# Optimization experiments

Hardware: AMD Instinct MI355X
Metric: run time of the kernel (lower is better)

The kernel has to match this reference:

```python
import jax, jax.numpy as jnp
import numpy as np

N_NODES = 100000
N_EDGES = 250000
D_NODE = 128
D_EDGE = 128
D_HID = 512
LN_EPS = 1e-5


def setup_inputs() -> dict:
    key = jax.random.key(0)
    ks = jax.random.split(key, 8)
    src_node_features = jax.random.normal(ks[0], (N_NODES, D_NODE), dtype=jnp.float32)
    dst_node_features = jax.random.normal(ks[1], (N_NODES, D_NODE), dtype=jnp.float32)
    edge_features = jax.random.normal(ks[2], (N_EDGES, D_EDGE), dtype=jnp.float32)
    src_indices = jax.random.randint(ks[3], (N_EDGES,), 0, N_NODES, dtype=jnp.int64 if jax.config.jax_enable_x64 else jnp.int32)
    dst_indices = jax.random.randint(ks[4], (N_EDGES,), 0, N_NODES, dtype=jnp.int64 if jax.config.jax_enable_x64 else jnp.int32)
    d_in = 2 * D_NODE + D_EDGE
    W1 = jax.random.normal(ks[5], (d_in, D_HID), dtype=jnp.float32) * (1.0 / np.sqrt(d_in))
    b1 = jnp.zeros((D_HID,), dtype=jnp.float32)
    W2 = jax.random.normal(ks[6], (D_HID, D_EDGE), dtype=jnp.float32) * (1.0 / np.sqrt(D_HID))
    b2 = jnp.zeros((D_EDGE,), dtype=jnp.float32)
    ln_gamma = jnp.ones((D_EDGE,), dtype=jnp.float32)
    ln_beta = jnp.zeros((D_EDGE,), dtype=jnp.float32)
    return {
        "src_node_features": src_node_features,
        "dst_node_features": dst_node_features,
        "edge_features": edge_features,
        "src_indices": src_indices,
        "dst_indices": dst_indices,
        "W1": W1, "b1": b1, "W2": W2, "b2": b2,
        "ln_gamma": ln_gamma, "ln_beta": ln_beta,
    }


def reference(src_node_features, dst_node_features, edge_features,
              src_indices, dst_indices, W1, b1, W2, b2, ln_gamma, ln_beta):
    # Gather node features per-edge (irregular access)
    s = src_node_features[src_indices]          # [E, D_NODE]
    d = dst_node_features[dst_indices]          # [E, D_NODE]
    x = jnp.concatenate([s, d, edge_features], axis=-1)  # [E, 2*D_NODE + D_EDGE]
    # MeshGraphMLP: Linear -> SiLU -> Linear -> LayerNorm
    h = jax.nn.silu(x @ W1 + b1)                # [E, D_HID]
    y = h @ W2 + b2                             # [E, D_EDGE]
    mu = jnp.mean(y, axis=-1, keepdims=True)
    var = jnp.var(y, axis=-1, keepdims=True)
    y = (y - mu) * jax.lax.rsqrt(var + LN_EPS) * ln_gamma + ln_beta
    # Residual add
    return y + edge_features
```

## Files before the change

kernel.cpp:

```cpp
#include <hip/hip_runtime.h>
#include <hip/hip_bf16.h>


typedef __bf16 bf16;
typedef __bf16 bf16x8 __attribute__((ext_vector_type(8)));
typedef float f32x4 __attribute__((ext_vector_type(4)));

#define E_TOT 250000
#define N_NODES 100000
#define ET 64
#define NBLK ((E_TOT + ET - 1) / ET)

__global__ __launch_bounds__(256) void pack_weights(const float* __restrict__ W1,
                                                    const float* __restrict__ W2,
                                                    bf16* __restrict__ W1p,
                                                    bf16* __restrict__ W2p) {
  int tid = blockIdx.x * blockDim.x + threadIdx.x;
  if (tid < 384 * 512) {
    int k = tid >> 9;
    int n = tid & 511;
    int kb = k >> 5, quad = (k >> 3) & 3, j = k & 7;
    W1p[(((kb * 4 + quad) * 512) + n) * 8 + j] = (bf16)W1[tid];
  }
  if (tid < 512 * 128) {
    int k = tid >> 7;
    int n = tid & 127;
    int kc = k >> 5, quad = (k >> 3) & 3, j = k & 7;
    W2p[(((kc * 4 + quad) * 128) + n) * 8 + j] = (bf16)W2[tid];
  }
}

__global__ __launch_bounds__(512, 4)
void edge_mlp_kernel(const float* __restrict__ srcf,
                     const float* __restrict__ dstf,
                     const float* __restrict__ edgef,
                     const int* __restrict__ sidx,
                     const int* __restrict__ didx,
                     const bf16* __restrict__ W1p,
                     const bf16* __restrict__ W2p,
                     const float* __restrict__ b1p,
                     const float* __restrict__ b2p,
                     const float* __restrict__ gp,
                     const float* __restrict__ bp,
                     float* __restrict__ out) {
  __shared__ __align__(16) bf16 Xs[48 * 512];
  __shared__ __align__(16) bf16 Hs[16 * 512];

  const int tid = threadIdx.x;
  const int w = tid >> 6;
  const int lane = tid & 63;
  const int l15 = lane & 15;
  const int quad = lane >> 4;
  const int h = w >> 2;
  const int q = w & 3;
  const long base = (long)blockIdx.x * ET;

  {
    const int mt = w & 3;
    const int half = w >> 2;
    int e = (int)base + mt * 16 + l15;
    int ec = e < E_TOT ? e : (E_TOT - 1);
    int si = sidx[ec];
    int di = didx[ec];
    si = si < 0 ? 0 : (si >= N_NODES ? N_NODES - 1 : si);
    di = di < 0 ? 0 : (di >= N_NODES ? N_NODES - 1 : di);
    const float* rs = srcf + (long)si * 128;
    const float* rd = dstf + (long)di * 128;
    const float* re = edgef + (long)ec * 128;
#pragma unroll
    for (int kk = 0; kk < 6; ++kk) {
      int kb = half * 6 + kk;
      const float* rowp = (kb < 4) ? rs : ((kb < 8) ? rd : re);
      int off = ((kb & 3) << 5) + (quad << 3);
      float4 v0 = *(const float4*)(rowp + off);
      float4 v1 = *(const float4*)(rowp + off + 4);
      bf16x8 vb;
      vb[0] = (bf16)v0.x; vb[1] = (bf16)v0.y; vb[2] = (bf16)v0.z; vb[3] = (bf16)v0.w;
      vb[4] = (bf16)v1.x; vb[5] = (bf16)v1.y; vb[6] = (bf16)v1.z; vb[7] = (bf16)v1.w;
      *(bf16x8*)(&Xs[(mt * 12 + kb) * 512 + lane * 8]) = vb;
    }
  }

  float b2v[2], gv[2], bv[2];
#pragma unroll
  for (int t = 0; t < 2; ++t) {
    int n2 = q * 32 + t * 16 + l15;
    b2v[t] = b2p[n2];
    gv[t] = gp[n2];
    bv[t] = bp[n2];
  }

  f32x4 acc2[2][2];
#pragma unroll
  for (int i = 0; i < 2; ++i)
#pragma unroll
    for (int t = 0; t < 2; ++t)
      acc2[i][t] = (f32x4){0.f, 0.f, 0.f, 0.f};

  __syncthreads();

  for (int nc = 0; nc < 4; ++nc) {
    f32x4 acc1[2][2];
#pragma unroll
    for (int i = 0; i < 2; ++i)
#pragma unroll
      for (int t = 0; t < 2; ++t)
        acc1[i][t] = (f32x4){0.f, 0.f, 0.f, 0.f};

    float b1v[2];
#pragma unroll
    for (int t = 0; t < 2; ++t)
      b1v[t] = b1p[nc * 128 + q * 32 + t * 16 + l15];

#pragma unroll
    for (int kb = 0; kb < 12; ++kb) {
      const bf16* wp = W1p + (((long)(kb * 4 + quad) * 512) + nc * 128 + q * 32) * 8;
      bf16x8 b[2];
      b[0] = *(const bf16x8*)(wp + l15 * 8);
      b[1] = *(const bf16x8*)(wp + (16 + l15) * 8);
      bf16x8 a[2];
#pragma unroll
      for (int i = 0; i < 2; ++i)
        a[i] = *(const bf16x8*)(&Xs[((h * 2 + i) * 12 + kb) * 512 + lane * 8]);
#pragma unroll
      for (int i = 0; i < 2; ++i)
#pragma unroll
        for (int t = 0; t < 2; ++t)
          acc1[i][t] =
              __builtin_amdgcn_mfma_f32_16x16x32_bf16(a[i], b[t], acc1[i][t], 0, 0, 0);
    }

    __syncthreads();

#pragma unroll
    for (int i = 0; i < 2; ++i)
#pragma unroll
      for (int t = 0; t < 2; ++t) {
        int pos0 = ((t * 2 + (l15 >> 3)) * 128) + (quad * 4) * 8 + (l15 & 7);
        bf16* hp = &Hs[((h * 2 + i) * 4 + q) * 512 + pos0];
#pragma unroll
        for (int r = 0; r < 4; ++r) {
          float vv = acc1[i][t][r] + b1v[t];
          float s = vv / (1.0f + __expf(-vv));
          hp[r * 8] = (bf16)s;
        }
      }
    __syncthreads();

#pragma unroll
    for (int kb2 = 0; kb2 < 4; ++kb2) {
      const bf16* wp =
          W2p + (((long)((nc * 4 + kb2) * 4 + quad) * 128) + q * 32) * 8;
      bf16x8 b[2];
      b[0] = *(const bf16x8*)(wp + l15 * 8);
      b[1] = *(const bf16x8*)(wp + (16 + l15) * 8);
      bf16x8 a[2];
#pragma unroll
      for (int i = 0; i < 2; ++i)
        a[i] = *(const bf16x8*)(&Hs[((h * 2 + i) * 4 + kb2) * 512 + lane * 8]);
#pragma unroll
      for (int i = 0; i < 2; ++i)
#pragma unroll
        for (int t = 0; t < 2; ++t)
          acc2[i][t] =
              __builtin_amdgcn_mfma_f32_16x16x32_bf16(a[i], b[t], acc2[i][t], 0, 0, 0);
    }
  }

  __syncthreads();

  float* psum = (float*)Hs;
  float* psq = psum + 256;
  float* pmu = psq + 256;
  float* prs = pmu + 64;

#pragma unroll
  for (int i = 0; i < 2; ++i) {
#pragma unroll
    for (int r = 0; r < 4; ++r) {
      float v0 = acc2[i][0][r] + b2v[0];
      float v1 = acc2[i][1][r] + b2v[1];
      float s = v0 + v1;
      float ss = v0 * v0 + v1 * v1;
#pragma unroll
      for (int mk = 8; mk >= 1; mk >>= 1) {
        s += __shfl_xor(s, mk, 64);
        ss += __shfl_xor(ss, mk, 64);
      }
      if (l15 == 0) {
        int row = (h * 2 + i) * 16 + quad * 4 + r;
        psum[row * 4 + q] = s;
        psq[row * 4 + q] = ss;
      }
    }
  }
  __syncthreads();
  if (tid < 64) {
    float s = psum[tid * 4] + psum[tid * 4 + 1] + psum[tid * 4 + 2] + psum[tid * 4 + 3];
    float ss = psq[tid * 4] + psq[tid * 4 + 1] + psq[tid * 4 + 2] + psq[tid * 4 + 3];
    float mu = s * (1.0f / 128.0f);
    float var = fmaxf(ss * (1.0f / 128.0f) - mu * mu, 0.0f);
    pmu[tid] = mu;
    prs[tid] = rsqrtf(var + 1e-5f);
  }
  __syncthreads();

#pragma unroll
  for (int i = 0; i < 2; ++i) {
#pragma unroll
    for (int r = 0; r < 4; ++r) {
      int m = (h * 2 + i) * 16 + quad * 4 + r;
      long e = base + m;
      if (e >= E_TOT) continue;
      float mu = pmu[m];
      float rsg = prs[m];
#pragma unroll
      for (int t = 0; t < 2; ++t) {
        int n2 = q * 32 + t * 16 + l15;
        float v = acc2[i][t][r] + b2v[t];
        int posE = ((t * 2 + (l15 >> 3)) * 128) + (quad * 4 + r) * 8 + (l15 & 7);
        float ev = (float)Xs[((h * 2 + i) * 12 + 8 + q) * 512 + posE];
        float y = (v - mu) * rsg * gv[t] + bv[t] + ev;
        out[e * 128 + n2] = y;
      }
    }
  }
}

extern "C" void kernel_launch(void* const* d_in, const int* in_sizes, int n_in,
                              void* d_out, int out_size, void* d_ws, size_t ws_size,
                              hipStream_t stream) {
  const float* srcf = (const float*)d_in[0];
  const float* dstf = (const float*)d_in[1];
  const float* edgef = (const float*)d_in[2];
  const int* sidx = (const int*)d_in[3];
  const int* didx = (const int*)d_in[4];
  const float* W1 = (const float*)d_in[5];
  const float* b1 = (const float*)d_in[6];
  const float* W2 = (const float*)d_in[7];
  const float* b2 = (const float*)d_in[8];
  const float* g = (const float*)d_in[9];
  const float* be = (const float*)d_in[10];
  float* out = (float*)d_out;

  bf16* W1p = (bf16*)d_ws;
  bf16* W2p = W1p + 384 * 512;

  pack_weights<<<(384 * 512 + 255) / 256, 256, 0, stream>>>(W1, W2, W1p, W2p);

  edge_mlp_kernel<<<NBLK, 512, 0, stream>>>(srcf, dstf, edgef, sidx, didx,
                                            W1p, W2p, b1, b2, g, be, out);
}
```

Measured before the change: 527.7 us.

## Double-buffer hidden tile in LDS and prefetch weight fragments ahead of MFMA

The hidden-activation LDS buffer is doubled so consecutive chunks alternate buffers, which lets one of the two barriers per chunk be removed. Weight fragments for both GEMMs are now loaded two k-steps ahead in a register ping-pong, so global load latency can overlap the MFMA work. This costs extra LDS, which may reduce occupancy, and extra registers for the prefetched fragments.

```diff
diff --git a/kernel.cpp b/kernel.cpp
--- a/kernel.cpp
+++ b/kernel.cpp
@@ -44,7 +44,7 @@
                      const float* __restrict__ bp,
                      float* __restrict__ out) {
   __shared__ __align__(16) bf16 Xs[48 * 512];
-  __shared__ __align__(16) bf16 Hs[16 * 512];
+  __shared__ __align__(16) bf16 Hs[2 * 16 * 512];
 
   const int tid = threadIdx.x;
   const int w = tid >> 6;
@@ -100,6 +100,8 @@
   __syncthreads();
 
   for (int nc = 0; nc < 4; ++nc) {
+    bf16* hbuf = &Hs[(nc & 1) * 16 * 512];
+
     f32x4 acc1[2][2];
 #pragma unroll
     for (int i = 0; i < 2; ++i)
@@ -112,12 +114,16 @@
     for (int t = 0; t < 2; ++t)
       b1v[t] = b1p[nc * 128 + q * 32 + t * 16 + l15];
 
+    bf16x8 bB[2][2];
+#pragma unroll
+    for (int p = 0; p < 2; ++p) {
+      const bf16* wp = W1p + (((long)(p * 4 + quad) * 512) + nc * 128 + q * 32) * 8;
+      bB[p][0] = *(const bf16x8*)(wp + l15 * 8);
+      bB[p][1] = *(const bf16x8*)(wp + (16 + l15) * 8);
+    }
+
 #pragma unroll
     for (int kb = 0; kb < 12; ++kb) {
-      const bf16* wp = W1p + (((long)(kb * 4 + quad) * 512) + nc * 128 + q * 32) * 8;
-      bf16x8 b[2];
-      b[0] = *(const bf16x8*)(wp + l15 * 8);
-      b[1] = *(const bf16x8*)(wp + (16 + l15) * 8);
       bf16x8 a[2];
 #pragma unroll
       for (int i = 0; i < 2; ++i)
@@ -126,18 +132,22 @@
       for (int i = 0; i < 2; ++i)
 #pragma unroll
         for (int t = 0; t < 2; ++t)
-          acc1[i][t] =
-              __builtin_amdgcn_mfma_f32_16x16x32_bf16(a[i], b[t], acc1[i][t], 0, 0, 0);
-    }
-
-    __syncthreads();
+          acc1[i][t] = __builtin_amdgcn_mfma_f32_16x16x32_bf16(a[i], bB[kb & 1][t],
+                                                              acc1[i][t], 0, 0, 0);
+      if (kb < 10) {
+        const bf16* wp =
+            W1p + (((long)((kb + 2) * 4 + quad) * 512) + nc * 128 + q * 32) * 8;
+        bB[kb & 1][0] = *(const bf16x8*)(wp + l15 * 8);
+        bB[kb & 1][1] = *(const bf16x8*)(wp + (16 + l15) * 8);
+      }
+    }
 
 #pragma unroll
     for (int i = 0; i < 2; ++i)
 #pragma unroll
       for (int t = 0; t < 2; ++t) {
         int pos0 = ((t * 2 + (l15 >> 3)) * 128) + (quad * 4) * 8 + (l15 & 7);
-        bf16* hp = &Hs[((h * 2 + i) * 4 + q) * 512 + pos0];
+        bf16* hp = &hbuf[((h * 2 + i) * 4 + q) * 512 + pos0];
 #pragma unroll
         for (int r = 0; r < 4; ++r) {
           float vv = acc1[i][t][r] + b1v[t];
@@ -147,23 +157,33 @@
       }
     __syncthreads();
 
+    bf16x8 bC[2][2];
+#pragma unroll
+    for (int p = 0; p < 2; ++p) {
+      const bf16* wp =
+          W2p + (((long)((nc * 4 + p) * 4 + quad) * 128) + q * 32) * 8;
+      bC[p][0] = *(const bf16x8*)(wp + l15 * 8);
+      bC[p][1] = *(const bf16x8*)(wp + (16 + l15) * 8);
+    }
+
 #pragma unroll
     for (int kb2 = 0; kb2 < 4; ++kb2) {
-      const bf16* wp =
-          W2p + (((long)((nc * 4 + kb2) * 4 + quad) * 128) + q * 32) * 8;
-      bf16x8 b[2];
-      b[0] = *(const bf16x8*)(wp + l15 * 8);
-      b[1] = *(const bf16x8*)(wp + (16 + l15) * 8);
       bf16x8 a[2];
 #pragma unroll
       for (int i = 0; i < 2; ++i)
-        a[i] = *(const bf16x8*)(&Hs[((h * 2 + i) * 4 + kb2) * 512 + lane * 8]);
+        a[i] = *(const bf16x8*)(&hbuf[((h * 2 + i) * 4 + kb2) * 512 + lane * 8]);
 #pragma unroll
       for (int i = 0; i < 2; ++i)
 #pragma unroll
         for (int t = 0; t < 2; ++t)
-          acc2[i][t] =
-              __builtin_amdgcn_mfma_f32_16x16x32_bf16(a[i], b[t], acc2[i][t], 0, 0, 0);
+          acc2[i][t] = __builtin_amdgcn_mfma_f32_16x16x32_bf16(a[i], bC[kb2 & 1][t],
+                                                              acc2[i][t], 0, 0, 0);
+      if (kb2 < 2) {
+        const bf16* wp =
+            W2p + (((long)((nc * 4 + kb2 + 2) * 4 + quad) * 128) + q * 32) * 8;
+        bC[kb2 & 1][0] = *(const bf16x8*)(wp + l15 * 8);
+        bC[kb2 & 1][1] = *(const bf16x8*)(wp + (16 + l15) * 8);
+      }
     }
   }
 
```

New measurement: 476.0 us. 9.8% less time.

## Double-buffer hidden tile and interleave second GEMM with next chunk's first GEMM

Applied to the files above, without the earlier changes.

Splits the hidden activation buffer into two halves so the second matmul of chunk nc-1 runs interleaved with the first matmul of chunk nc. This removes two of the three barriers per chunk. Weight fragments are prefetched into registers one or two steps ahead. SiLU now uses a hardware reciprocal instead of a divide. The cost is more LDS and registers, which could reduce occupancy.

```diff
diff --git a/kernel.cpp b/kernel.cpp
--- a/kernel.cpp
+++ b/kernel.cpp
@@ -29,6 +29,52 @@
     W2p[(((kc * 4 + quad) * 128) + n) * 8 + j] = (bf16)W2[tid];
   }
 }
+
+#define MFMA16(a, b, c) __builtin_amdgcn_mfma_f32_16x16x32_bf16(a, b, c, 0, 0, 0)
+
+#define G1_STEP(kb, nc)                                                       \
+  do {                                                                        \
+    bf16x8 a0_ = *(const bf16x8*)(&Xs[((h * 2 + 0) * 12 + (kb)) * 512 + lane * 8]); \
+    bf16x8 a1_ = *(const bf16x8*)(&Xs[((h * 2 + 1) * 12 + (kb)) * 512 + lane * 8]); \
+    acc1[0][0] = MFMA16(a0_, bB[(kb)&1][0], acc1[0][0]);                      \
+    acc1[0][1] = MFMA16(a0_, bB[(kb)&1][1], acc1[0][1]);                      \
+    acc1[1][0] = MFMA16(a1_, bB[(kb)&1][0], acc1[1][0]);                      \
+    acc1[1][1] = MFMA16(a1_, bB[(kb)&1][1], acc1[1][1]);                      \
+    if ((kb) < 10) {                                                          \
+      const bf16* wp_ = W1base + ((long)((kb) + 2) * 16384 + (long)(nc)*1024); \
+      bB[(kb)&1][0] = *(const bf16x8*)(wp_);                                  \
+      bB[(kb)&1][1] = *(const bf16x8*)(wp_ + 128);                            \
+    }                                                                         \
+  } while (0)
+
+#define G2_STEP(kb2, nc2, hb)                                                 \
+  do {                                                                        \
+    bf16x8 a0_ = *(const bf16x8*)(&(hb)[((h * 2 + 0) * 4 + (kb2)) * 512 + lane * 8]); \
+    bf16x8 a1_ = *(const bf16x8*)(&(hb)[((h * 2 + 1) * 4 + (kb2)) * 512 + lane * 8]); \
+    acc2[0][0] = MFMA16(a0_, bC[(kb2)&1][0], acc2[0][0]);                     \
+    acc2[0][1] = MFMA16(a0_, bC[(kb2)&1][1], acc2[0][1]);                     \
+    acc2[1][0] = MFMA16(a1_, bC[(kb2)&1][0], acc2[1][0]);                     \
+    acc2[1][1] = MFMA16(a1_, bC[(kb2)&1][1], acc2[1][1]);                     \
+    if ((kb2) < 2) {                                                          \
+      const bf16* wp_ = W2base + ((long)((nc2)*4 + (kb2) + 2) * 4096);        \
+      bC[(kb2)&1][0] = *(const bf16x8*)(wp_);                                 \
+      bC[(kb2)&1][1] = *(const bf16x8*)(wp_ + 128);                           \
+    }                                                                         \
+  } while (0)
+
+#define SCATTER(hb)                                                           \
+  do {                                                                        \
+    _Pragma("unroll") for (int i_ = 0; i_ < 2; ++i_)                          \
+    _Pragma("unroll") for (int t_ = 0; t_ < 2; ++t_) {                        \
+      int pos0_ = ((t_ * 2 + (l15 >> 3)) * 128) + (quad * 4) * 8 + (l15 & 7); \
+      bf16* hp_ = &(hb)[((h * 2 + i_) * 4 + q) * 512 + pos0_];                \
+      _Pragma("unroll") for (int r_ = 0; r_ < 4; ++r_) {                      \
+        float vv_ = acc1[i_][t_][r_] + b1v[t_];                               \
+        float s_ = vv_ * __builtin_amdgcn_rcpf(1.0f + __expf(-vv_));          \
+        hp_[r_ * 8] = (bf16)s_;                                               \
+      }                                                                       \
+    }                                                                         \
+  } while (0)
 
 __global__ __launch_bounds__(512, 4)
 void edge_mlp_kernel(const float* __restrict__ srcf,
@@ -44,7 +90,7 @@
                      const float* __restrict__ bp,
                      float* __restrict__ out) {
   __shared__ __align__(16) bf16 Xs[48 * 512];
-  __shared__ __align__(16) bf16 Hs[16 * 512];
+  __shared__ __align__(16) bf16 Hs[2 * 16 * 512];
 
   const int tid = threadIdx.x;
   const int w = tid >> 6;
@@ -90,84 +136,95 @@
     bv[t] = bp[n2];
   }
 
-  f32x4 acc2[2][2];
+  const bf16* W1base = W1p + ((long)quad * 512 + q * 32 + l15) * 8;
+  const bf16* W2base = W2p + ((long)quad * 128 + q * 32 + l15) * 8;
+
+  f32x4 acc1[2][2], acc2[2][2];
+  bf16x8 bB[2][2], bC[2][2];
+  float b1v[2];
+
 #pragma unroll
   for (int i = 0; i < 2; ++i)
 #pragma unroll
-    for (int t = 0; t < 2; ++t)
+    for (int t = 0; t < 2; ++t) {
+      acc1[i][t] = (f32x4){0.f, 0.f, 0.f, 0.f};
       acc2[i][t] = (f32x4){0.f, 0.f, 0.f, 0.f};
+    }
+
+#pragma unroll
+  for (int p = 0; p < 2; ++p) {
+    const bf16* wp_ = W1base + (long)p * 16384;
+    bB[p][0] = *(const bf16x8*)(wp_);
+    bB[p][1] = *(const bf16x8*)(wp_ + 128);
+  }
+  b1v[0] = b1p[q * 32 + l15];
+  b1v[1] = b1p[q * 32 + 16 + l15];
 
   __syncthreads();
 
-  for (int nc = 0; nc < 4; ++nc) {
-    f32x4 acc1[2][2];
+  G1_STEP(0, 0);  G1_STEP(1, 0);  G1_STEP(2, 0);  G1_STEP(3, 0);
+  G1_STEP(4, 0);  G1_STEP(5, 0);  G1_STEP(6, 0);  G1_STEP(7, 0);
+  G1_STEP(8, 0);  G1_STEP(9, 0);  G1_STEP(10, 0); G1_STEP(11, 0);
+
+#pragma unroll
+  for (int p = 0; p < 2; ++p) {
+    const bf16* wp1 = W1base + ((long)p * 16384 + 1024);
+    bB[p][0] = *(const bf16x8*)(wp1);
+    bB[p][1] = *(const bf16x8*)(wp1 + 128);
+    const bf16* wp2 = W2base + (long)p * 4096;
+    bC[p][0] = *(const bf16x8*)(wp2);
+    bC[p][1] = *(const bf16x8*)(wp2 + 128);
+  }
+
+  SCATTER(&Hs[0]);
+  __syncthreads();
+
+#pragma unroll
+  for (int nc = 1; nc < 4; ++nc) {
+    bf16* hprev = &Hs[((nc - 1) & 1) * 16 * 512];
+    bf16* hcur = &Hs[(nc & 1) * 16 * 512];
+    b1v[0] = b1p[nc * 128 + q * 32 + l15];
+    b1v[1] = b1p[nc * 128 + q * 32 + 16 + l15];
 #pragma unroll
     for (int i = 0; i < 2; ++i)
 #pragma unroll
-      for (int t = 0; t < 2; ++t)
-        acc1[i][t] = (f32x4){0.f, 0.f, 0.f, 0.f};
-
-    float b1v[2];
-#pragma unroll
-    for (int t = 0; t < 2; ++t)
-      b1v[t] = b1p[nc * 128 + q * 32 + t * 16 + l15];
-
-#pragma unroll
-    for (int kb = 0; kb < 12; ++kb) {
-      const bf16* wp = W1p + (((long)(kb * 4 + quad) * 512) + nc * 128 + q * 32) * 8;
-      bf16x8 b[2];
-      b[0] = *(const bf16x8*)(wp + l15 * 8);
-      b[1] = *(const bf16x8*)(wp + (16 + l15) * 8);
-      bf16x8 a[2];
-#pragma unroll
-      for (int i = 0; i < 2; ++i)
-        a[i] = *(const bf16x8*)(&Xs[((h * 2 + i) * 12 + kb) * 512 + lane * 8]);
-#pragma unroll
-      for (int i = 0; i < 2; ++i)
-#pragma unroll
-        for (int t = 0; t < 2; ++t)
-          acc1[i][t] =
-              __builtin_amdgcn_mfma_f32_16x16x32_bf16(a[i], b[t], acc1[i][t], 0, 0, 0);
-    }
-
+      for (int t = 0; t < 2; ++t) acc1[i][t] = (f32x4){0.f, 0.f, 0.f, 0.f};
+
+    G1_STEP(0, nc);  G1_STEP(1, nc);  G1_STEP(2, nc);  G2_STEP(0, nc - 1, hprev);
+    G1_STEP(3, nc);  G1_STEP(4, nc);  G1_STEP(5, nc);  G2_STEP(1, nc - 1, hprev);
+    G1_STEP(6, nc);  G1_STEP(7, nc);  G1_STEP(8, nc);  G2_STEP(2, nc - 1, hprev);
+    G1_STEP(9, nc);  G1_STEP(10, nc); G1_STEP(11, nc); G2_STEP(3, nc - 1, hprev);
+
+    if (nc < 3) {
+#pragma unroll
+      for (int p = 0; p < 2; ++p) {
+        const bf16* wp1 = W1base + ((long)p * 16384 + (long)(nc + 1) * 1024);
+        bB[p][0] = *(const bf16x8*)(wp1);
+        bB[p][1] = *(const bf16x8*)(wp1 + 128);
+        const bf16* wp2 = W2base + ((long)(nc * 4 + p)) * 4096;
+        bC[p][0] = *(const bf16x8*)(wp2);
+        bC[p][1] = *(const bf16x8*)(wp2 + 128);
+      }
+    } else {
+#pragma unroll
+      for (int p = 0; p < 2; ++p) {
+        const bf16* wp2 = W2base + ((long)(12 + p)) * 4096;
+        bC[p][0] = *(const bf16x8*)(wp2);
+        bC[p][1] = *(const bf16x8*)(wp2 + 128);
+      }
+    }
+
+    SCATTER(hcur);
     __syncthreads();
-
-#pragma unroll
-    for (int i = 0; i < 2; ++i)
-#pragma unroll
-      for (int t = 0; t < 2; ++t) {
-        int pos0 = ((t * 2 + (l15 >> 3)) * 128) + (quad * 4) * 8 + (l15 & 7);
-        bf16* hp = &Hs[((h * 2 + i) * 4 + q) * 512 + pos0];
-#pragma unroll
-        for (int r = 0; r < 4; ++r) {
-          float vv = acc1[i][t][r] + b1v[t];
-          float s = vv / (1.0f + __expf(-vv));
-          hp[r * 8] = (bf16)s;
-        }
-      }
-    __syncthreads();
-
-#pragma unroll
-    for (int kb2 = 0; kb2 < 4; ++kb2) {
-      const bf16* wp =
-          W2p + (((long)((nc * 4 + kb2) * 4 + quad) * 128) + q * 32) * 8;
-      bf16x8 b[2];
-      b[0] = *(const bf16x8*)(wp + l15 * 8);
-      b[1] = *(const bf16x8*)(wp + (16 + l15) * 8);
-      bf16x8 a[2];
-#pragma unroll
-      for (int i = 0; i < 2; ++i)
-        a[i] = *(const bf16x8*)(&Hs[((h * 2 + i) * 4 + kb2) * 512 + lane * 8]);
-#pragma unroll
-      for (int i = 0; i < 2; ++i)
-#pragma unroll
-        for (int t = 0; t < 2; ++t)
-          acc2[i][t] =
-              __builtin_amdgcn_mfma_f32_16x16x32_bf16(a[i], b[t], acc2[i][t], 0, 0, 0);
-    }
-  }
-
-  __syncthreads();
+  }
+
+  {
+    bf16* hb3 = &Hs[1 * 16 * 512];
+    G2_STEP(0, 3, hb3);
+    G2_STEP(1, 3, hb3);
+    G2_STEP(2, 3, hb3);
+    G2_STEP(3, 3, hb3);
+  }
 
   float* psum = (float*)Hs;
   float* psq = psum + 256;
```

New measurement: 486.3 us. 1.09x faster.
